# Kernel optimization log

Hardware: AMD Instinct MI355X
Metric: run time of the kernel (lower is better)

The kernel has to match this reference:

```python
import jax, jax.numpy as jnp
import numpy as np

B, S, H = 1, 2048, 2048
I = 1408
E = 64
TOP_K = 8
N_GROUP = 8
TOPK_GROUP = 4
SCALE = 2.5
N_SHARED = 2


def setup_inputs() -> dict:
    key = jax.random.key(0)
    ks = jax.random.split(key, 9)
    x = jax.random.normal(ks[0], (B, S, H), dtype=jnp.float32)
    # kaiming_uniform(a=sqrt(5)) for [E, H] weight -> bound = 1/sqrt(H)
    gate_w = jax.random.uniform(ks[1], (E, H), jnp.float32, -1.0, 1.0) / jnp.sqrt(float(H))
    e_bias = jnp.zeros((E,), jnp.float32)
    gate_proj = jax.random.normal(ks[2], (E, I, H), jnp.float32) * 0.02
    up_proj = jax.random.normal(ks[3], (E, I, H), jnp.float32) * 0.02
    down_proj = jax.random.normal(ks[4], (E, H, I), jnp.float32) * 0.02
    SI = I * N_SHARED
    shared_gate_w = jax.random.uniform(ks[5], (SI, H), jnp.float32, -1.0, 1.0) / jnp.sqrt(float(H))
    shared_up_w = jax.random.uniform(ks[6], (SI, H), jnp.float32, -1.0, 1.0) / jnp.sqrt(float(H))
    shared_down_w = jax.random.uniform(ks[7], (H, SI), jnp.float32, -1.0, 1.0) / jnp.sqrt(float(SI))
    return {"hidden_states": x, "gate_w": gate_w, "e_bias": e_bias,
            "gate_proj": gate_proj, "up_proj": up_proj, "down_proj": down_proj,
            "shared_gate_w": shared_gate_w, "shared_up_w": shared_up_w,
            "shared_down_w": shared_down_w}


def _moe_forward(hidden_states, gate_w, e_bias, gate_proj, up_proj, down_proj,
                 shared_gate_w, shared_up_w, shared_down_w):
    bsz, seq_len, h = hidden_states.shape
    xf = hidden_states.reshape(-1, h).astype(jnp.float32)  # [T, H]
    T = bsz * seq_len

    # ---- DeepSeek group-restricted top-k gating ----
    logits = xf @ gate_w.T                                  # [T, E]
    scores = jax.nn.sigmoid(logits)
    scores_for_choice = scores + e_bias[None, :]
    gs = scores_for_choice.reshape(T, N_GROUP, E // N_GROUP)
    group_scores = jax.lax.top_k(gs, 2)[0].sum(-1)          # [T, n_group] sum of top-2 per group
    group_idx = jax.lax.top_k(group_scores, TOPK_GROUP)[1]  # [T, topk_group]
    group_mask = jax.nn.one_hot(group_idx, N_GROUP, dtype=jnp.float32).sum(1)  # [T, n_group]
    score_mask = jnp.repeat(group_mask, E // N_GROUP, axis=1)                  # [T, E]
    tmp_scores = jnp.where(score_mask > 0, scores_for_choice, 0.0)
    topk_idx = jax.lax.top_k(tmp_scores, TOP_K)[1]          # [T, top_k]
    topk_w = jnp.take_along_axis(scores, topk_idx, axis=1)  # gather from UN-biased scores
    topk_w = topk_w / (topk_w.sum(-1, keepdims=True) + 1e-20)
    topk_w = topk_w * SCALE

    # Dense combine weights [T, E]; exactly equivalent to sort/dispatch/combine.
    rows = jnp.arange(T)
    cw = jnp.zeros((T, E), jnp.float32).at[rows[:, None], topk_idx].add(topk_w)

    # ---- per-expert FFN, accumulated with lax.scan over the (fixed) expert axis ----
    def step(y, we):
        Wg, Wu, Wd, w = we                                  # [I,H],[I,H],[H,I],[T]
        g = xf @ Wg.T                                       # [T, I]
        u = xf @ Wu.T
        inter = jax.nn.silu(g) * u                          # silu_mul kernel
        out = inter @ Wd.T                                  # [T, H]
        return y + out * w[:, None], None

    y0 = jnp.zeros_like(xf)
    y, _ = jax.lax.scan(step, y0, (gate_proj, up_proj, down_proj, cw.T))
    y = y.reshape(bsz, seq_len, h)

    # ---- shared experts ----
    sg = hidden_states @ shared_gate_w.T                    # [B, S, SI]
    su = hidden_states @ shared_up_w.T
    shared_out = (jax.nn.silu(sg) * su) @ shared_down_w.T   # [B, S, H]
    return y + shared_out


def reference(hidden_states, gate_w, e_bias, gate_proj, up_proj, down_proj,
              shared_gate_w, shared_up_w, shared_down_w):
    return _moe_forward(hidden_states, gate_w, e_bias, gate_proj, up_proj, down_proj,
                        shared_gate_w, shared_up_w, shared_down_w)
```

## Files before the change

kernel.cpp:

```cpp
#include <hip/hip_runtime.h>

typedef unsigned short u16;
typedef unsigned int u32;
typedef __attribute__((ext_vector_type(8))) short short8;
typedef __attribute__((ext_vector_type(8))) u16 ushort8;
typedef __attribute__((ext_vector_type(4))) float f32x4;

#define T_TOK 2048
#define H_DIM 2048
#define NEXP 64
#define I_DIM 1408
#define SI_DIM 2816
#define BM 128
#define BK 64
#define MAXT 256

__device__ __forceinline__ u16 f2bf(float f) {
    u32 u = __builtin_bit_cast(u32, f);
    u32 r = u + 0x7FFFu + ((u >> 16) & 1u);
    return (u16)(r >> 16);
}

__device__ __forceinline__ ushort8 cvt8(f32x4 a, f32x4 b) {
    ushort8 o;
    o[0] = f2bf(a[0]); o[1] = f2bf(a[1]); o[2] = f2bf(a[2]); o[3] = f2bf(a[3]);
    o[4] = f2bf(b[0]); o[5] = f2bf(b[1]); o[6] = f2bf(b[2]); o[7] = f2bf(b[3]);
    return o;
}

__device__ __forceinline__ f32x4 mfma16(short8 a, short8 b, f32x4 c) {
    return __builtin_amdgcn_mfma_f32_16x16x32_bf16(a, b, c, 0, 0, 0);
}

__global__ __launch_bounds__(256) void k_cvt(const float* __restrict__ x, u16* __restrict__ xb) {
    int i = (blockIdx.x * 256 + threadIdx.x) * 8;
    f32x4 v0 = *(const f32x4*)(x + i);
    f32x4 v1 = *(const f32x4*)(x + i + 4);
    *(ushort8*)(xb + i) = cvt8(v0, v1);
}

__global__ __launch_bounds__(256) void k_gate_logits(const float* __restrict__ x,
        const float* __restrict__ gw, float* __restrict__ logits) {
    __shared__ float xs[8][65];
    __shared__ float wsh[64][65];
    int tid = threadIdx.x;
    int t0 = blockIdx.x * 8;
    double acc0 = 0.0, acc1 = 0.0;
    int e = tid & 63, tg = tid >> 6;
    for (int k0 = 0; k0 < H_DIM; k0 += 64) {
        #pragma unroll
        for (int s = 0; s < 2; ++s) {
            int idx = s * 256 + tid;
            int r = idx >> 6, k = idx & 63;
            xs[r][k] = x[(size_t)(t0 + r) * H_DIM + k0 + k];
        }
        #pragma unroll
        for (int s = 0; s < 16; ++s) {
            int idx = s * 256 + tid;
            int r = idx >> 6, k = idx & 63;
            wsh[r][k] = gw[(size_t)r * H_DIM + k0 + k];
        }
        __syncthreads();
        #pragma unroll 8
        for (int k = 0; k < 64; ++k) {
            double wv = (double)wsh[e][k];
            acc0 += (double)xs[tg][k] * wv;
            acc1 += (double)xs[tg + 4][k] * wv;
        }
        __syncthreads();
    }
    logits[(size_t)(t0 + tg) * NEXP + e] = (float)acc0;
    logits[(size_t)(t0 + tg + 4) * NEXP + e] = (float)acc1;
}

__global__ __launch_bounds__(256) void k_topk(const float* __restrict__ logits,
        const float* __restrict__ ebias, int* __restrict__ topk_idx,
        float* __restrict__ topk_w, int* __restrict__ counts) {
    __shared__ float bsh[64];
    if (threadIdx.x < 64) bsh[threadIdx.x] = ebias[threadIdx.x];
    __syncthreads();
    int t = blockIdx.x * 256 + threadIdx.x;
    float sc[64];
    #pragma unroll
    for (int e2 = 0; e2 < 64; ++e2) {
        float lg = logits[(size_t)t * 64 + e2];
        sc[e2] = 1.0f / (1.0f + expf(-lg));
    }
    float gsc[8];
    #pragma unroll
    for (int g = 0; g < 8; ++g) {
        float m1 = -1e30f, m2 = -1e30f;
        #pragma unroll
        for (int j = 0; j < 8; ++j) {
            float v = sc[g * 8 + j] + bsh[g * 8 + j];
            if (v > m1) { m2 = m1; m1 = v; }
            else if (v > m2) { m2 = v; }
        }
        gsc[g] = m1 + m2;
    }
    u32 gmask = 0;
    #pragma unroll
    for (int it = 0; it < 4; ++it) {
        float best = -1e30f; int bi = 0;
        #pragma unroll
        for (int g = 0; g < 8; ++g) {
            bool ok = !((gmask >> g) & 1u);
            if (ok && gsc[g] > best) { best = gsc[g]; bi = g; }
        }
        gmask |= 1u << bi;
    }
    unsigned long long avail = 0ull;
    #pragma unroll
    for (int g = 0; g < 8; ++g)
        if ((gmask >> g) & 1u) avail |= (0xFFull << (g * 8));
    float wsum = 0.f;
    int idx[8]; float wv[8];
    #pragma unroll
    for (int it = 0; it < 8; ++it) {
        float best = -1e30f, bw = 0.f; int bi = 0;
        #pragma unroll
        for (int e2 = 0; e2 < 64; ++e2) {
            bool ok = (avail >> e2) & 1ull;
            float v = sc[e2] + bsh[e2];
            if (ok && v > best) { best = v; bi = e2; bw = sc[e2]; }
        }
        avail &= ~(1ull << bi);
        idx[it] = bi; wv[it] = bw; wsum += bw;
    }
    float scale = 2.5f / (wsum + 1e-20f);
    #pragma unroll
    for (int it = 0; it < 8; ++it) {
        topk_idx[t * 8 + it] = idx[it];
        topk_w[t * 8 + it] = wv[it] * scale;
        atomicAdd(&counts[idx[it]], 1);
    }
}

__global__ void k_prefix(const int* __restrict__ counts, int* __restrict__ offsets,
                         int* __restrict__ tiles, int* __restrict__ ntiles) {
    if (threadIdx.x == 0) {
        int run = 0;
        for (int e = 0; e < 64; ++e) { offsets[e] = run; run += counts[e]; }
        offsets[64] = run;
        for (int i = 0; i < MAXT; ++i) tiles[i] = -1;
        int slot[8] = {0, 0, 0, 0, 0, 0, 0, 0};
        int nt = 0;
        for (int e = 0; e < 64; ++e) {
            int xcd = e & 7;
            int c = counts[e];
            for (int m0 = 0; m0 < c; m0 += BM) {
                int pos = xcd + 8 * slot[xcd];
                if (pos < MAXT) { tiles[pos] = (e << 16) | m0; slot[xcd]++; nt++; }
            }
        }
        *ntiles = nt;
    }
}

__global__ __launch_bounds__(256) void k_scatter(const int* __restrict__ topk_idx,
        const float* __restrict__ topk_w, const int* __restrict__ offsets,
        int* __restrict__ fill, int* __restrict__ tok_list, float* __restrict__ w_list) {
    int gid = blockIdx.x * 256 + threadIdx.x;
    int t = gid >> 3;
    int e = topk_idx[gid];
    int pos = offsets[e] + atomicAdd(&fill[e], 1);
    tok_list[pos] = t;
    w_list[pos] = topk_w[gid];
}

__global__ __launch_bounds__(256, 2) void k_gateup(
        const u16* __restrict__ xb,
        const float* __restrict__ gate_base, const float* __restrict__ up_base,
        const int* __restrict__ offsets, const int* __restrict__ tok_list,
        const int* __restrict__ tiles, const int* __restrict__ ntiles,
        u16* __restrict__ inter, int Irows) {
    int e, m0, seg, n, i0;
    if (tiles) {
        int tt = tiles[blockIdx.x];
        if (tt < 0) return;
        e = tt >> 16; m0 = tt & 0xFFFF;
        seg = offsets[e]; n = offsets[e + 1] - seg;
        i0 = blockIdx.y * 64;
    } else {
        e = 0; seg = 0; n = T_TOK;
        i0 = blockIdx.x * 64;
        if (i0 >= Irows) return;
        m0 = blockIdx.y * BM;
    }
    if (n <= 0 || m0 >= n) return;

    const float* Bg = gate_base + (size_t)e * Irows * H_DIM;
    const float* Bu = up_base + (size_t)e * Irows * H_DIM;

    __shared__ u16 As[2][BM * BK];
    __shared__ u16 Bsg[2][64 * BK];
    __shared__ u16 Bsu[2][64 * BK];

    int tid = threadIdx.x;
    int w = tid >> 6, lane = tid & 63;

    const u16* asrc[4]; int adst[4];
    #pragma unroll
    for (int s = 0; s < 4; ++s) {
        int slot = s * 256 + tid;
        int r = slot >> 3, cb = slot & 7;
        int p = m0 + r; if (p >= n) p = n - 1;
        int tok = tok_list ? tok_list[seg + p] : p;
        asrc[s] = xb + (size_t)tok * H_DIM + cb * 8;
        adst[s] = r * BK + ((cb ^ (r & 7)) * 8);
    }
    const float* bgsrc[2]; const float* busrc[2]; int bdst[2];
    #pragma unroll
    for (int s = 0; s < 2; ++s) {
        int slot = s * 256 + tid;
        int r = slot >> 3, cb = slot & 7;
        bgsrc[s] = Bg + (size_t)(i0 + r) * H_DIM + cb * 8;
        busrc[s] = Bu + (size_t)(i0 + r) * H_DIM + cb * 8;
        bdst[s] = r * BK + ((cb ^ (r & 7)) * 8);
    }

    f32x4 zero; zero[0] = 0.f; zero[1] = 0.f; zero[2] = 0.f; zero[3] = 0.f;
    f32x4 accg[2][4], accu[2][4];
    #pragma unroll
    for (int a = 0; a < 2; ++a)
        #pragma unroll
        for (int b = 0; b < 4; ++b) { accg[a][b] = zero; accu[a][b] = zero; }

    short8 stA[4];
    f32x4 stG[2][2], stU[2][2];

    auto ldregs = [&](int k0) {
        #pragma unroll
        for (int s = 0; s < 4; ++s) stA[s] = *(const short8*)(asrc[s] + k0);
        #pragma unroll
        for (int s = 0; s < 2; ++s) {
            stG[s][0] = *(const f32x4*)(bgsrc[s] + k0);
            stG[s][1] = *(const f32x4*)(bgsrc[s] + k0 + 4);
            stU[s][0] = *(const f32x4*)(busrc[s] + k0);
            stU[s][1] = *(const f32x4*)(busrc[s] + k0 + 4);
        }
    };
    auto dswrite = [&](int buf) {
        #pragma unroll
        for (int s = 0; s < 4; ++s) *(ushort8*)(&As[buf][adst[s]]) = *(const ushort8*)&stA[s];
        #pragma unroll
        for (int s = 0; s < 2; ++s) {
            *(ushort8*)(&Bsg[buf][bdst[s]]) = cvt8(stG[s][0], stG[s][1]);
            *(ushort8*)(&Bsu[buf][bdst[s]]) = cvt8(stU[s][0], stU[s][1]);
        }
    };
    auto mmaStep = [&](int buf) {
        #pragma unroll
        for (int ks = 0; ks < 2; ++ks) {
            short8 a[2];
            #pragma unroll
            for (int fm = 0; fm < 2; ++fm) {
                int row = w * 32 + fm * 16 + (lane & 15);
                int cb = ks * 4 + (lane >> 4);
                a[fm] = *(const short8*)(&As[buf][row * BK + ((cb ^ (row & 7)) * 8)]);
            }
            #pragma unroll
            for (int fn = 0; fn < 4; ++fn) {
                int brow = fn * 16 + (lane & 15);
                int cb = ks * 4 + (lane >> 4);
                int boff = brow * BK + ((cb ^ (brow & 7)) * 8);
                short8 bg = *(const short8*)(&Bsg[buf][boff]);
                short8 bu = *(const short8*)(&Bsu[buf][boff]);
                accg[0][fn] = mfma16(a[0], bg, accg[0][fn]);
                accg[1][fn] = mfma16(a[1], bg, accg[1][fn]);
                accu[0][fn] = mfma16(a[0], bu, accu[0][fn]);
                accu[1][fn] = mfma16(a[1], bu, accu[1][fn]);
            }
        }
    };

    const int NK = H_DIM / BK;
    ldregs(0);
    dswrite(0);
    __syncthreads();
    for (int t = 0; t < NK; ++t) {
        if (t + 1 < NK) ldregs((t + 1) * BK);
        mmaStep(t & 1);
        if (t + 1 < NK) dswrite((t + 1) & 1);
        __syncthreads();
    }

    int r0 = (lane >> 4) * 4, cc = lane & 15;
    #pragma unroll
    for (int fm = 0; fm < 2; ++fm) {
        #pragma unroll
        for (int r = 0; r < 4; ++r) {
            int p = m0 + w * 32 + fm * 16 + r0 + r;
            if (p < n) {
                size_t rowb = (size_t)(seg + p) * Irows + i0;
                #pragma unroll
                for (int fn = 0; fn < 4; ++fn) {
                    float g = accg[fm][fn][r], u = accu[fm][fn][r];
                    float val = g / (1.0f + expf(-g)) * u;
                    inter[rowb + fn * 16 + cc] = f2bf(val);
                }
            }
        }
    }
}

__global__ __launch_bounds__(256, 2) void k_down(
        const u16* __restrict__ inter, int Kdim,
        const float* __restrict__ down_base,
        const int* __restrict__ offsets, const int* __restrict__ tok_list,
        const int* __restrict__ tiles, const int* __restrict__ ntiles,
        const float* __restrict__ w_list,
        float* __restrict__ out) {
    int e, m0, seg, n, h0;
    if (tiles) {
        int tt = tiles[blockIdx.x];
        if (tt < 0) return;
        e = tt >> 16; m0 = tt & 0xFFFF;
        seg = offsets[e]; n = offsets[e + 1] - seg;
        h0 = blockIdx.y * 128;
    } else {
        e = 0; seg = 0; n = T_TOK;
        h0 = blockIdx.x * 128;
        m0 = blockIdx.y * BM;
    }
    if (n <= 0 || m0 >= n) return;

    const float* Bd = down_base + (size_t)e * H_DIM * Kdim;

    __shared__ u16 As[2][BM * BK];
    __shared__ u16 Bs[2][128 * BK];

    int tid = threadIdx.x;
    int w = tid >> 6, lane = tid & 63;

    const u16* asrc[4]; int adst[4];
    #pragma unroll
    for (int s = 0; s < 4; ++s) {
        int slot = s * 256 + tid;
        int r = slot >> 3, cb = slot & 7;
        int p = m0 + r; if (p >= n) p = n - 1;
        asrc[s] = inter + (size_t)(seg + p) * Kdim + cb * 8;
        adst[s] = r * BK + ((cb ^ (r & 7)) * 8);
    }
    const float* bsrc[4]; int bdst[4];
    #pragma unroll
    for (int s = 0; s < 4; ++s) {
        int slot = s * 256 + tid;
        int r = slot >> 3, cb = slot & 7;
        bsrc[s] = Bd + (size_t)(h0 + r) * Kdim + cb * 8;
        bdst[s] = r * BK + ((cb ^ (r & 7)) * 8);
    }

    f32x4 zero; zero[0] = 0.f; zero[1] = 0.f; zero[2] = 0.f; zero[3] = 0.f;
    f32x4 acc[2][8];
    #pragma unroll
    for (int a = 0; a < 2; ++a)
        #pragma unroll
        for (int b = 0; b < 8; ++b) acc[a][b] = zero;

    short8 stA[4];
    f32x4 stB[4][2];

    auto ldregs = [&](int k0) {
        #pragma unroll
        for (int s = 0; s < 4; ++s) stA[s] = *(const short8*)(asrc[s] + k0);
        #pragma unroll
        for (int s = 0; s < 4; ++s) {
            stB[s][0] = *(const f32x4*)(bsrc[s] + k0);
            stB[s][1] = *(const f32x4*)(bsrc[s] + k0 + 4);
        }
    };
    auto dswrite = [&](int buf) {
        #pragma unroll
        for (int s = 0; s < 4; ++s) *(ushort8*)(&As[buf][adst[s]]) = *(const ushort8*)&stA[s];
        #pragma unroll
        for (int s = 0; s < 4; ++s)
            *(ushort8*)(&Bs[buf][bdst[s]]) = cvt8(stB[s][0], stB[s][1]);
    };
    auto mmaStep = [&](int buf) {
        #pragma unroll
        for (int ks = 0; ks < 2; ++ks) {
            short8 a[2];
            #pragma unroll
            for (int fm = 0; fm < 2; ++fm) {
                int row = w * 32 + fm * 16 + (lane & 15);
                int cb = ks * 4 + (lane >> 4);
                a[fm] = *(const short8*)(&As[buf][row * BK + ((cb ^ (row & 7)) * 8)]);
            }
            #pragma unroll
            for (int fn = 0; fn < 8; ++fn) {
                int brow = fn * 16 + (lane & 15);
                int cb = ks * 4 + (lane >> 4);
                short8 b = *(const short8*)(&Bs[buf][brow * BK + ((cb ^ (brow & 7)) * 8)]);
                acc[0][fn] = mfma16(a[0], b, acc[0][fn]);
                acc[1][fn] = mfma16(a[1], b, acc[1][fn]);
            }
        }
    };

    const int NK = Kdim / BK;
    ldregs(0);
    dswrite(0);
    __syncthreads();
    for (int t = 0; t < NK; ++t) {
        if (t + 1 < NK) ldregs((t + 1) * BK);
        mmaStep(t & 1);
        if (t + 1 < NK) dswrite((t + 1) & 1);
        __syncthreads();
    }

    int r0 = (lane >> 4) * 4, cc = lane & 15;
    #pragma unroll
    for (int fm = 0; fm < 2; ++fm) {
        #pragma unroll
        for (int r = 0; r < 4; ++r) {
            int p = m0 + w * 32 + fm * 16 + r0 + r;
            if (p < n) {
                int tok = tok_list ? tok_list[seg + p] : p;
                size_t ob = (size_t)tok * H_DIM + h0 + cc;
                if (w_list) {
                    float wt = w_list[seg + p];
                    #pragma unroll
                    for (int fn = 0; fn < 8; ++fn)
                        atomicAdd(&out[ob + fn * 16], acc[fm][fn][r] * wt);
                } else {
                    #pragma unroll
                    for (int fn = 0; fn < 8; ++fn)
                        out[ob + fn * 16] = acc[fm][fn][r];
                }
            }
        }
    }
}

extern "C" void kernel_launch(void* const* d_in, const int* in_sizes, int n_in,
                              void* d_out, int out_size, void* d_ws, size_t ws_size,
                              hipStream_t stream) {
    const float* x         = (const float*)d_in[0];
    const float* gate_w    = (const float*)d_in[1];
    const float* e_bias    = (const float*)d_in[2];
    const float* gate_proj = (const float*)d_in[3];
    const float* up_proj   = (const float*)d_in[4];
    const float* down_proj = (const float*)d_in[5];
    const float* sgw       = (const float*)d_in[6];
    const float* suw       = (const float*)d_in[7];
    const float* sdw       = (const float*)d_in[8];
    float* out = (float*)d_out;

    char* ws = (char*)d_ws;
    size_t off = 0;
    auto alloc = [&](size_t bytes) -> char* {
        char* p = ws + off;
        off += (bytes + 255) & ~(size_t)255;
        return p;
    };
    float* logits   = (float*)alloc((size_t)T_TOK * 64 * 4);
    int*   topk_idx = (int*)  alloc((size_t)T_TOK * 8 * 4);
    float* topk_w   = (float*)alloc((size_t)T_TOK * 8 * 4);
    int*   counts   = (int*)  alloc(256);
    int*   offsets  = (int*)  alloc(512);
    int*   fill     = (int*)  alloc(256);
    int*   tiles    = (int*)  alloc(MAXT * 4);
    int*   ntiles   = (int*)  alloc(256);
    int*   tok_list = (int*)  alloc((size_t)T_TOK * 8 * 4);
    float* w_list   = (float*)alloc((size_t)T_TOK * 8 * 4);
    u16*   xb       = (u16*)  alloc((size_t)T_TOK * H_DIM * 2);
    u16*   inter    = (u16*)  alloc((size_t)T_TOK * 8 * I_DIM * 2);

    hipMemsetAsync(counts, 0, 1024, stream);

    k_cvt<<<(T_TOK * H_DIM) / 2048, 256, 0, stream>>>(x, xb);
    k_gate_logits<<<T_TOK / 8, 256, 0, stream>>>(x, gate_w, logits);
    k_topk<<<T_TOK / 256, 256, 0, stream>>>(logits, e_bias, topk_idx, topk_w, counts);
    k_prefix<<<1, 64, 0, stream>>>(counts, offsets, tiles, ntiles);
    k_scatter<<<(T_TOK * 8) / 256, 256, 0, stream>>>(topk_idx, topk_w, offsets, fill, tok_list, w_list);

    k_gateup<<<dim3(48, T_TOK / BM), 256, 0, stream>>>(
        xb, sgw, suw, nullptr, nullptr, nullptr, nullptr, inter, SI_DIM);
    k_down<<<dim3(16, T_TOK / BM), 256, 0, stream>>>(
        inter, SI_DIM, sdw, nullptr, nullptr, nullptr, nullptr, nullptr, out);

    k_gateup<<<dim3(MAXT, I_DIM / 64), 256, 0, stream>>>(
        xb, gate_proj, up_proj, offsets, tok_list, tiles, ntiles, inter, I_DIM);
    k_down<<<dim3(MAXT, H_DIM / 128), 256, 0, stream>>>(
        inter, I_DIM, down_proj, offsets, tok_list, tiles, ntiles, w_list, out);
}
```

Baseline: 1.311 ms.

## Deepen global-load prefetch to two stages in expert GEMM kernels

Both the gate/up and down GEMM kernels now keep two register staging sets, so global loads for tile t+2 are issued while tile t is multiplied. Before, only tile t+1 was in flight. This gives global memory latency more time to hide behind MFMA work. It roughly doubles the staging register footprint, which may lower occupancy or cause spills. MAXT is also raised from 256 to 384, which changes the per-expert token capacity and possibly the launch grid.

```diff
diff --git a/kernel.cpp b/kernel.cpp
--- a/kernel.cpp
+++ b/kernel.cpp
@@ -13,7 +13,7 @@
 #define SI_DIM 2816
 #define BM 128
 #define BK 64
-#define MAXT 256
+#define MAXT 384
 
 __device__ __forceinline__ u16 f2bf(float f) {
     u32 u = __builtin_bit_cast(u32, f);
@@ -226,27 +226,49 @@
         #pragma unroll
         for (int b = 0; b < 4; ++b) { accg[a][b] = zero; accu[a][b] = zero; }
 
-    short8 stA[4];
-    f32x4 stG[2][2], stU[2][2];
-
-    auto ldregs = [&](int k0) {
-        #pragma unroll
-        for (int s = 0; s < 4; ++s) stA[s] = *(const short8*)(asrc[s] + k0);
+    short8 stA0[4], stA1[4];
+    f32x4 stG0[2][2], stU0[2][2], stG1[2][2], stU1[2][2];
+
+    auto ldS0 = [&](int t) {
+        int k0 = t * BK;
+        #pragma unroll
+        for (int s = 0; s < 4; ++s) stA0[s] = *(const short8*)(asrc[s] + k0);
         #pragma unroll
         for (int s = 0; s < 2; ++s) {
-            stG[s][0] = *(const f32x4*)(bgsrc[s] + k0);
-            stG[s][1] = *(const f32x4*)(bgsrc[s] + k0 + 4);
-            stU[s][0] = *(const f32x4*)(busrc[s] + k0);
-            stU[s][1] = *(const f32x4*)(busrc[s] + k0 + 4);
-        }
-    };
-    auto dswrite = [&](int buf) {
-        #pragma unroll
-        for (int s = 0; s < 4; ++s) *(ushort8*)(&As[buf][adst[s]]) = *(const ushort8*)&stA[s];
+            stG0[s][0] = *(const f32x4*)(bgsrc[s] + k0);
+            stG0[s][1] = *(const f32x4*)(bgsrc[s] + k0 + 4);
+            stU0[s][0] = *(const f32x4*)(busrc[s] + k0);
+            stU0[s][1] = *(const f32x4*)(busrc[s] + k0 + 4);
+        }
+    };
+    auto ldS1 = [&](int t) {
+        int k0 = t * BK;
+        #pragma unroll
+        for (int s = 0; s < 4; ++s) stA1[s] = *(const short8*)(asrc[s] + k0);
         #pragma unroll
         for (int s = 0; s < 2; ++s) {
-            *(ushort8*)(&Bsg[buf][bdst[s]]) = cvt8(stG[s][0], stG[s][1]);
-            *(ushort8*)(&Bsu[buf][bdst[s]]) = cvt8(stU[s][0], stU[s][1]);
+            stG1[s][0] = *(const f32x4*)(bgsrc[s] + k0);
+            stG1[s][1] = *(const f32x4*)(bgsrc[s] + k0 + 4);
+            stU1[s][0] = *(const f32x4*)(busrc[s] + k0);
+            stU1[s][1] = *(const f32x4*)(busrc[s] + k0 + 4);
+        }
+    };
+    auto dsw0 = [&]() {
+        #pragma unroll
+        for (int s = 0; s < 4; ++s) *(ushort8*)(&As[0][adst[s]]) = *(const ushort8*)&stA0[s];
+        #pragma unroll
+        for (int s = 0; s < 2; ++s) {
+            *(ushort8*)(&Bsg[0][bdst[s]]) = cvt8(stG0[s][0], stG0[s][1]);
+            *(ushort8*)(&Bsu[0][bdst[s]]) = cvt8(stU0[s][0], stU0[s][1]);
+        }
+    };
+    auto dsw1 = [&]() {
+        #pragma unroll
+        for (int s = 0; s < 4; ++s) *(ushort8*)(&As[1][adst[s]]) = *(const ushort8*)&stA1[s];
+        #pragma unroll
+        for (int s = 0; s < 2; ++s) {
+            *(ushort8*)(&Bsg[1][bdst[s]]) = cvt8(stG1[s][0], stG1[s][1]);
+            *(ushort8*)(&Bsu[1][bdst[s]]) = cvt8(stU1[s][0], stU1[s][1]);
         }
     };
     auto mmaStep = [&](int buf) {
@@ -275,14 +297,20 @@
     };
 
     const int NK = H_DIM / BK;
-    ldregs(0);
-    dswrite(0);
+    ldS0(0); dsw0();
+    ldS1(1);
     __syncthreads();
-    for (int t = 0; t < NK; ++t) {
-        if (t + 1 < NK) ldregs((t + 1) * BK);
-        mmaStep(t & 1);
-        if (t + 1 < NK) dswrite((t + 1) & 1);
+    for (int t = 0; t < NK; t += 2) {
+        if (t + 2 < NK) ldS0(t + 2);
+        mmaStep(0);
+        if (t + 1 < NK) dsw1();
         __syncthreads();
+        if (t + 1 < NK) {
+            if (t + 3 < NK) ldS1(t + 3);
+            mmaStep(1);
+            if (t + 2 < NK) dsw0();
+            __syncthreads();
+        }
     }
 
     int r0 = (lane >> 4) * 4, cc = lane & 15;
@@ -358,24 +386,42 @@
         #pragma unroll
         for (int b = 0; b < 8; ++b) acc[a][b] = zero;
 
-    short8 stA[4];
-    f32x4 stB[4][2];
-
-    auto ldregs = [&](int k0) {
-        #pragma unroll
-        for (int s = 0; s < 4; ++s) stA[s] = *(const short8*)(asrc[s] + k0);
+    short8 stA0[4], stA1[4];
+    f32x4 stB0[4][2], stB1[4][2];
+
+    auto ldS0 = [&](int t) {
+        int k0 = t * BK;
+        #pragma unroll
+        for (int s = 0; s < 4; ++s) stA0[s] = *(const short8*)(asrc[s] + k0);
         #pragma unroll
         for (int s = 0; s < 4; ++s) {
-            stB[s][0] = *(const f32x4*)(bsrc[s] + k0);
-            stB[s][1] = *(const f32x4*)(bsrc[s] + k0 + 4);
-        }
-    };
-    auto dswrite = [&](int buf) {
-        #pragma unroll
-        for (int s = 0; s < 4; ++s) *(ushort8*)(&As[buf][adst[s]]) = *(const ushort8*)&stA[s];
+            stB0[s][0] = *(const f32x4*)(bsrc[s] + k0);
+            stB0[s][1] = *(const f32x4*)(bsrc[s] + k0 + 4);
+        }
+    };
+    auto ldS1 = [&](int t) {
+        int k0 = t * BK;
+        #pragma unroll
+        for (int s = 0; s < 4; ++s) stA1[s] = *(const short8*)(asrc[s] + k0);
+        #pragma unroll
+        for (int s = 0; s < 4; ++s) {
+            stB1[s][0] = *(const f32x4*)(bsrc[s] + k0);
+            stB1[s][1] = *(const f32x4*)(bsrc[s] + k0 + 4);
+        }
+    };
+    auto dsw0 = [&]() {
+        #pragma unroll
+        for (int s = 0; s < 4; ++s) *(ushort8*)(&As[0][adst[s]]) = *(const ushort8*)&stA0[s];
         #pragma unroll
         for (int s = 0; s < 4; ++s)
-            *(ushort8*)(&Bs[buf][bdst[s]]) = cvt8(stB[s][0], stB[s][1]);
+            *(ushort8*)(&Bs[0][bdst[s]]) = cvt8(stB0[s][0], stB0[s][1]);
+    };
+    auto dsw1 = [&]() {
+        #pragma unroll
+        for (int s = 0; s < 4; ++s) *(ushort8*)(&As[1][adst[s]]) = *(const ushort8*)&stA1[s];
+        #pragma unroll
+        for (int s = 0; s < 4; ++s)
+            *(ushort8*)(&Bs[1][bdst[s]]) = cvt8(stB1[s][0], stB1[s][1]);
     };
     auto mmaStep = [&](int buf) {
         #pragma unroll
@@ -399,14 +445,20 @@
     };
 
     const int NK = Kdim / BK;
-    ldregs(0);
-    dswrite(0);
+    ldS0(0); dsw0();
+    ldS1(1);
     __syncthreads();
-    for (int t = 0; t < NK; ++t) {
-        if (t + 1 < NK) ldregs((t + 1) * BK);
-        mmaStep(t & 1);
-        if (t + 1 < NK) dswrite((t + 1) & 1);
+    for (int t = 0; t < NK; t += 2) {
+        if (t + 2 < NK) ldS0(t + 2);
+        mmaStep(0);
+        if (t + 1 < NK) dsw1();
         __syncthreads();
+        if (t + 1 < NK) {
+            if (t + 3 < NK) ldS1(t + 3);
+            mmaStep(1);
+            if (t + 2 < NK) dsw0();
+            __syncthreads();
+        }
     }
 
     int r0 = (lane >> 4) * 4, cc = lane & 15;
```

New measurement: 1.301 ms. Within noise of the previous version (-0.8%).
